# Kernel tuning notes

Hardware: AMD Instinct MI355X
Metric: run time of the kernel (lower is better)

The kernel has to match this reference:

```python
import jax, jax.numpy as jnp
import numpy as np
import math

UNIT = 46
KEY_SIZE = 16
MAX_POS = 50
NEG_BIG = 1.0e12


def _rope_tables(max_pos, d):
    pos = np.arange(max_pos, dtype=np.float32)[:, None]
    div = np.exp(np.arange(0, d, 2, dtype=np.float32) * (-math.log(10000.0) / d))
    sin = np.sin(pos * div)  # [P, d/2]
    cos = np.cos(pos * div)  # [P, d/2]
    # matches torch repeat_interleave(2, dim=-1) of the strided sinusoid table
    cos_rep = np.repeat(cos, 2, axis=-1)  # [P, d]
    sin_rep = np.repeat(sin, 2, axis=-1)  # [P, d]
    return jnp.asarray(cos_rep), jnp.asarray(sin_rep)

_COS, _SIN = _rope_tables(MAX_POS, KEY_SIZE)


def _apply_rope(qw):
    # qw: [B, S, d]
    s = qw.shape[-2]
    qw2 = jnp.stack([-qw[..., 1::2], qw[..., ::2]], axis=-1).reshape(qw.shape)
    return qw * _COS[:s] + qw2 * _SIN[:s]


def setup_inputs() -> dict:
    key = jax.random.key(0)
    ks = jax.random.split(key, 8)
    B, S = 32768, 50
    x = jax.random.normal(ks[0], (B, S, UNIT), dtype=jnp.float32)
    mask = jnp.ones((B, S), dtype=jnp.float32)
    d_in = UNIT
    sc = 1.0 / math.sqrt(d_in)
    Wi = jax.random.uniform(ks[1], (2 * UNIT + KEY_SIZE, d_in), minval=-sc, maxval=sc, dtype=jnp.float32)
    bi = jax.random.uniform(ks[2], (2 * UNIT + KEY_SIZE,), minval=-sc, maxval=sc, dtype=jnp.float32)
    Wo = jax.random.uniform(ks[3], (UNIT, UNIT), minval=-sc, maxval=sc, dtype=jnp.float32)
    bo = jax.random.uniform(ks[4], (UNIT,), minval=-sc, maxval=sc, dtype=jnp.float32)
    Wq = jax.random.uniform(ks[5], (1, UNIT), minval=-sc, maxval=sc, dtype=jnp.float32)
    bq = jax.random.uniform(ks[6], (1,), minval=-sc, maxval=sc, dtype=jnp.float32)
    scale_q = jnp.ones((KEY_SIZE,), jnp.float32)
    offset_q = jnp.zeros((KEY_SIZE,), jnp.float32)
    scale_k = jnp.ones((KEY_SIZE,), jnp.float32)
    offset_k = jnp.zeros((KEY_SIZE,), jnp.float32)
    return {"x": x, "mask": mask, "Wi": Wi, "bi": bi, "Wo": Wo, "bo": bo,
            "scale_q": scale_q, "offset_q": offset_q, "scale_k": scale_k,
            "offset_k": offset_k, "Wq": Wq, "bq": bq}


def reference(x, mask, Wi, bi, Wo, bo, scale_q, offset_q, scale_k, offset_k, Wq, bq):
    # x: [B, S, U], mask: [B, S]
    h = jax.nn.silu(jnp.einsum('bsu,ou->bso', x, Wi) + bi)  # [B, S, 2U+K]
    u, v, qk = jnp.split(h, [UNIT, 2 * UNIT], axis=-1)
    q = _apply_rope(qk * scale_q + offset_q)  # [B, S, K]
    k = _apply_rope(qk * scale_k + offset_k)  # [B, S, K]
    A = jnp.einsum('bik,bjk->bij', q, k) / math.sqrt(KEY_SIZE)  # [B, S, S]
    m = mask[:, None, :]
    A = jax.nn.softmax(A * m + (1.0 - m) * (-NEG_BIG), axis=-1)
    # NOTE: original overwrites the gated output with a plain matmul (u unused)
    out = jnp.einsum('bij,bju->biu', A, v)  # [B, S, U]
    out = jnp.einsum('biu,ou->bio', out, Wo) + bo  # [B, S, U]
    prob = (jnp.einsum('bsu,ou->bso', out, Wq) + bq)[..., 0]  # [B, S]
    prob = prob * mask - (1.0 - mask) * NEG_BIG
    prob = jax.nn.softmax(prob, axis=-1)
    return jnp.sum(out * prob[..., None], axis=1)  # [B, U]
```

## Files before the change

### kernel.cpp

```cpp
#include <hip/hip_runtime.h>
#include <math.h>

#define SEQ 50
#define UNITD 46
#define NEGBIG 1000000000000.0f

typedef _Float16 f16;
typedef f16 f16x4 __attribute__((ext_vector_type(4)));
typedef f16 f16x8 __attribute__((ext_vector_type(8)));
typedef float f32x4 __attribute__((ext_vector_type(4)));
typedef unsigned u32x2 __attribute__((ext_vector_type(2)));
typedef unsigned u32x4 __attribute__((ext_vector_type(4)));

__device__ __forceinline__ float rcpf(float x) { return __builtin_amdgcn_rcpf(x); }
__device__ __forceinline__ unsigned pk2(float lo, float hi) {
    return __builtin_bit_cast(unsigned, __builtin_amdgcn_cvt_pkrtz(lo, hi));
}

#define ARENA 12800
#define QOFF 0
#define KOFF 2560
#define VOFF 6400
#define MOFF 12544

__device__ __forceinline__ int swzP(int row, int colbyte) {
    return row * 128 + (colbyte ^ ((row & 7) << 4));
}
__device__ __forceinline__ int swzV(int row, int colbyte) {
    return VOFF + row * 128 + (colbyte ^ ((row & 7) << 4));
}

#define WS_ROPE 14336

__global__ void prep_kernel(const float* __restrict__ Wi,
                            const float* __restrict__ Wo,
                            char* __restrict__ ws)
{
    f16x8* wf = (f16x8*)ws;
    const int lane = threadIdx.x & 63;
    const int g = lane >> 4, t = lane & 15;
    #pragma unroll
    for (int nt = 0; nt < 4; ++nt) {
        int c = t + 16 * nt; bool cok = c < 62;
        const float* wr = Wi + (size_t)(UNITD + (cok ? c : 0)) * UNITD;
        #pragma unroll
        for (int kt = 0; kt < 2; ++kt) {
            f16x8 f;
            #pragma unroll
            for (int jj = 0; jj < 8; ++jj) {
                int u = 32 * kt + 8 * g + jj;
                f[jj] = (f16)((cok && u < UNITD) ? wr[u] : 0.f);
            }
            wf[(nt * 2 + kt) * 64 + lane] = f;
        }
    }
    #pragma unroll
    for (int mo = 0; mo < 3; ++mo) {
        int o = 16 * mo + t; bool ook = o < UNITD;
        const float* wr = Wo + (size_t)(ook ? o : 0) * UNITD;
        #pragma unroll
        for (int kt = 0; kt < 2; ++kt) {
            f16x8 f;
            #pragma unroll
            for (int jj = 0; jj < 8; ++jj) {
                int u = 32 * kt + 8 * g + jj;
                f[jj] = (f16)((ook && u < UNITD) ? wr[u] : 0.f);
            }
            wf[512 + (mo * 2 + kt) * 64 + lane] = f;
        }
    }
    {
        float2* rt = (float2*)(ws + WS_ROPE);
        int seq = threadIdx.x;
        #pragma unroll
        for (int d = 0; d < 16; ++d) {
            float ang = (float)seq * expf(-(float)(d >> 1) * 1.1512925464970229f);
            float sn, cs;
            sincosf(ang, &sn, &cs);
            float2 v; v.x = cs * 0.5f; v.y = ((d & 1) ? sn : -sn) * 0.5f;
            rt[seq * 16 + d] = v;
        }
    }
}

__global__ __launch_bounds__(256, 3) void gau_kernel(
    const float* __restrict__ x,
    const float* __restrict__ mask,
    const char* __restrict__ ws,
    const float* __restrict__ bi,
    const float* __restrict__ bo,
    const float* __restrict__ sq,
    const float* __restrict__ oq,
    const float* __restrict__ sk,
    const float* __restrict__ ok,
    const float* __restrict__ Wq,
    const float* __restrict__ bq,
    float* __restrict__ out,
    int Btot)
{
    const int lane = threadIdx.x & 63;
    const int wid  = threadIdx.x >> 6;
    const int b    = blockIdx.x * 4 + wid;
    const int g    = lane >> 4;
    const int t    = lane & 15;

    const f16x8* wf = (const f16x8*)ws;

    __shared__ __align__(16) char smem[4 * ARENA];
    char* wa = smem + wid * ARENA;
    float* M = (float*)(wa + MOFF);

    if (b >= Btot) return;

    M[lane] = (lane < SEQ) ? mask[(size_t)b * SEQ + lane] : 0.f;

    f16x8 bfW[4][2];
    float biv[4];
    #pragma unroll
    for (int nt = 0; nt < 4; ++nt) {
        int c = t + 16 * nt;
        biv[nt] = (c < 62) ? bi[UNITD + c] : 0.f;
        #pragma unroll
        for (int kt = 0; kt < 2; ++kt)
            bfW[nt][kt] = wf[(nt * 2 + kt) * 64 + lane];
    }

    f32x4 hB[4][4];
    #pragma unroll
    for (int mt = 0; mt < 4; ++mt)
        #pragma unroll
        for (int nt = 0; nt < 4; ++nt) {
            f32x4 c; c[0] = biv[nt]; c[1] = biv[nt]; c[2] = biv[nt]; c[3] = biv[nt];
            hB[mt][nt] = c;
        }

    const float* xb = x + (size_t)b * (SEQ * UNITD);
    #pragma unroll
    for (int mt = 0; mt < 4; ++mt) {
        int row = 16 * mt + t; if (row > SEQ - 1) row = SEQ - 1;
        const float* xr = xb + row * UNITD;
        #pragma unroll
        for (int kt = 0; kt < 2; ++kt) {
            u32x4 axw;
            #pragma unroll
            for (int jj2 = 0; jj2 < 4; ++jj2) {
                int u = 32 * kt + 8 * g + 2 * jj2;
                float lo = 0.f, hi = 0.f;
                if (u < UNITD) { float2 w = *(const float2*)(xr + u); lo = w.x; hi = w.y; }
                axw[jj2] = pk2(lo, hi);
            }
            f16x8 ax = __builtin_bit_cast(f16x8, axw);
            #pragma unroll
            for (int nt = 0; nt < 4; ++nt)
                hB[mt][nt] = __builtin_amdgcn_mfma_f32_16x16x32_f16(ax, bfW[nt][kt], hB[mt][nt], 0, 0, 0);
        }
    }

    float qkv[4][4];
    #pragma unroll
    for (int mt = 0; mt < 4; ++mt) {
        float s2[4], s3[4];
        #pragma unroll
        for (int nt = 0; nt < 4; ++nt) {
            float sl[4];
            #pragma unroll
            for (int r = 0; r < 4; ++r) {
                float h = hB[mt][nt][r];
                sl[r] = h * rcpf(1.f + __expf(-h));
            }
            int ucol = t + 16 * nt;
            if (nt < 3 && ucol < UNITD) {
                u32x2 pw; pw[0] = pk2(sl[0], sl[1]); pw[1] = pk2(sl[2], sl[3]);
                *(f16x4*)(wa + swzV(ucol, (16 * mt + 4 * g) * 2)) = __builtin_bit_cast(f16x4, pw);
            }
            if (nt == 2) { s2[0]=sl[0]; s2[1]=sl[1]; s2[2]=sl[2]; s2[3]=sl[3]; }
            if (nt == 3) { s3[0]=sl[0]; s3[1]=sl[1]; s3[2]=sl[2]; s3[3]=sl[3]; }
        }
        #pragma unroll
        for (int r = 0; r < 4; ++r) qkv[mt][r] = (t >= 14) ? s2[r] : s3[r];
    }

    {
        f16* Q = (f16*)(wa + QOFF);
        f16* K = (f16*)(wa + KOFF);
        const float2* rt = (const float2*)(ws + WS_ROPE);
        int d = (t >= 14) ? (t - 14) : (t + 2);
        float sqd = sq[d], oqd = oq[d], skd = sk[d], okd = ok[d];
        #pragma unroll
        for (int mt = 0; mt < 4; ++mt)
            #pragma unroll
            for (int r = 0; r < 4; ++r) {
                int seq = 16 * mt + 4 * g + r;
                float2 cn = rt[seq * 16 + d];
                float qv = qkv[mt][r] * sqd + oqd;
                float kv = qkv[mt][r] * skd + okd;
                float qp = __shfl_xor(qv, 1);
                float kp = __shfl_xor(kv, 1);
                Q[seq * 20 + d] = (f16)(qv * cn.x + qp * cn.y);
                K[seq * 20 + d] = (f16)(kv * cn.x + kp * cn.y);
            }
    }

    f16x4 ak[4], bq_[4];
    #pragma unroll
    for (int m4 = 0; m4 < 4; ++m4) ak[m4]  = *(f16x4*)(wa + KOFF + (16 * m4 + t) * 40 + 8 * g);
    #pragma unroll
    for (int n4 = 0; n4 < 4; ++n4) bq_[n4] = *(f16x4*)(wa + QOFF + (16 * n4 + t) * 40 + 8 * g);

    f32x4 pT[4][4];
    #pragma unroll
    for (int m4 = 0; m4 < 4; ++m4)
        #pragma unroll
        for (int n4 = 0; n4 < 4; ++n4) {
            f32x4 z; z[0]=0.f; z[1]=0.f; z[2]=0.f; z[3]=0.f;
            pT[m4][n4] = __builtin_amdgcn_mfma_f32_16x16x16f16(ak[m4], bq_[n4], z, 0, 0, 0);
        }

    f32x4 mj4[4];
    float NBv[4][4];
    #pragma unroll
    for (int m4 = 0; m4 < 4; ++m4) {
        mj4[m4] = *(f32x4*)(M + 16 * m4 + 4 * g);
        #pragma unroll
        for (int r = 0; r < 4; ++r)
            NBv[m4][r] = fmaf(mj4[m4][r], NEGBIG, -NEGBIG);
    }

    #pragma unroll
    for (int n4 = 0; n4 < 4; ++n4) {
        float a_[4][4];
        #pragma unroll
        for (int m4 = 0; m4 < 4; ++m4)
            #pragma unroll
            for (int r = 0; r < 4; ++r)
                a_[m4][r] = fmaf(pT[m4][n4][r], mj4[m4][r], NBv[m4][r]);

        float mr[4];
        #pragma unroll
        for (int m4 = 0; m4 < 4; ++m4)
            mr[m4] = fmaxf(fmaxf(a_[m4][0], a_[m4][1]), fmaxf(a_[m4][2], a_[m4][3]));
        float mx = fmaxf(fmaxf(mr[0], mr[1]), fmaxf(mr[2], mr[3]));
        mx = fmaxf(mx, __shfl_xor(mx, 16)); mx = fmaxf(mx, __shfl_xor(mx, 32));

        float sr[4];
        #pragma unroll
        for (int m4 = 0; m4 < 4; ++m4) {
            #pragma unroll
            for (int r = 0; r < 4; ++r) a_[m4][r] = __expf(a_[m4][r] - mx);
            sr[m4] = (a_[m4][0] + a_[m4][1]) + (a_[m4][2] + a_[m4][3]);
        }
        float sm = (sr[0] + sr[1]) + (sr[2] + sr[3]);
        sm += __shfl_xor(sm, 16); sm += __shfl_xor(sm, 32);
        float inv = rcpf(sm);

        int i = t + 16 * n4;
        if (i < SEQ) {
            #pragma unroll
            for (int m4 = 0; m4 < 4; ++m4) {
                u32x2 pw;
                pw[0] = pk2(a_[m4][0] * inv, a_[m4][1] * inv);
                pw[1] = pk2(a_[m4][2] * inv, a_[m4][3] * inv);
                *(f16x4*)(wa + swzP(i, (16 * m4 + 4 * g) * 2)) = __builtin_bit_cast(f16x4, pw);
            }
        }
    }

    f16x8 bv[3][2];
    #pragma unroll
    for (int nt = 0; nt < 3; ++nt)
        #pragma unroll
        for (int kt = 0; kt < 2; ++kt)
            bv[nt][kt] = *(f16x8*)(wa + swzV(t + 16 * nt, (32 * kt + 8 * g) * 2));

    f32x4 oA[4][3];
    #pragma unroll
    for (int mt = 0; mt < 4; ++mt)
        #pragma unroll
        for (int nt = 0; nt < 3; ++nt) { f32x4 z; z[0]=0.f; z[1]=0.f; z[2]=0.f; z[3]=0.f; oA[mt][nt] = z; }

    #pragma unroll
    for (int mt = 0; mt < 4; ++mt) {
        int pr = 16 * mt + t; if (pr > SEQ - 1) pr = SEQ - 1;
        #pragma unroll
        for (int kt = 0; kt < 2; ++kt) {
            f16x8 ap = *(f16x8*)(wa + swzP(pr, (32 * kt + 8 * g) * 2));
            #pragma unroll
            for (int nt = 0; nt < 3; ++nt)
                oA[mt][nt] = __builtin_amdgcn_mfma_f32_16x16x32_f16(ap, bv[nt][kt], oA[mt][nt], 0, 0, 0);
        }
    }

    #pragma unroll
    for (int mt = 0; mt < 4; ++mt)
        #pragma unroll
        for (int nt = 0; nt < 3; ++nt) {
            int u = t + 16 * nt;
            if (u < UNITD) {
                #pragma unroll
                for (int r = 0; r < 4; ++r) {
                    int i = 4 * g + r + 16 * mt;
                    if (i < SEQ)
                        *(f16*)(wa + swzP(i, u * 2)) = (f16)oA[mt][nt][r];
                }
            }
        }

    f16x8 aw[3][2];
    #pragma unroll
    for (int mo = 0; mo < 3; ++mo)
        #pragma unroll
        for (int kt = 0; kt < 2; ++kt)
            aw[mo][kt] = wf[512 + (mo * 2 + kt) * 64 + lane];

    float bov[3][4], wqv[3][4];
    #pragma unroll
    for (int mo = 0; mo < 3; ++mo)
        #pragma unroll
        for (int r = 0; r < 4; ++r) {
            int o = 16 * mo + 4 * g + r; bool ok2 = (o < UNITD);
            bov[mo][r] = ok2 ? bo[o] : 0.f;
            wqv[mo][r] = ok2 ? Wq[o] : 0.f;
        }

    f32x4 o2[3][4];
    #pragma unroll
    for (int mo = 0; mo < 3; ++mo)
        #pragma unroll
        for (int n4 = 0; n4 < 4; ++n4) {
            f32x4 c;
            #pragma unroll
            for (int r = 0; r < 4; ++r) c[r] = bov[mo][r];
            o2[mo][n4] = c;
        }

    #pragma unroll
    for (int n4 = 0; n4 < 4; ++n4) {
        int br = t + 16 * n4; if (br > SEQ - 1) br = SEQ - 1;
        #pragma unroll
        for (int kt = 0; kt < 2; ++kt) {
            f16x8 bo_ = *(f16x8*)(wa + swzP(br, (32 * kt + 8 * g) * 2));
            #pragma unroll
            for (int mo = 0; mo < 3; ++mo)
                o2[mo][n4] = __builtin_amdgcn_mfma_f32_16x16x32_f16(aw[mo][kt], bo_, o2[mo][n4], 0, 0, 0);
        }
    }

    float bq0 = bq[0];
    float tv[4]; float mx2 = -INFINITY;
    #pragma unroll
    for (int n4 = 0; n4 < 4; ++n4) {
        float s = 0.f;
        #pragma unroll
        for (int mo = 0; mo < 3; ++mo)
            #pragma unroll
            for (int r = 0; r < 4; ++r) s += o2[mo][n4][r] * wqv[mo][r];
        s += __shfl_xor(s, 16); s += __shfl_xor(s, 32);
        float mi = M[t + 16 * n4];
        float nb = fmaf(mi, NEGBIG, -NEGBIG);
        tv[n4] = fmaf(s + bq0, mi, nb);
        mx2 = fmaxf(mx2, tv[n4]);
    }
    #pragma unroll
    for (int off = 1; off <= 8; off <<= 1) mx2 = fmaxf(mx2, __shfl_xor(mx2, off));
    float sm2 = 0.f;
    #pragma unroll
    for (int n4 = 0; n4 < 4; ++n4) { float e = __expf(tv[n4] - mx2); tv[n4] = e; sm2 += e; }
    #pragma unroll
    for (int off = 1; off <= 8; off <<= 1) sm2 += __shfl_xor(sm2, off);
    float inv2 = rcpf(sm2);

    #pragma unroll
    for (int mo = 0; mo < 3; ++mo) {
        float racc[4];
        #pragma unroll
        for (int r = 0; r < 4; ++r) {
            float a = 0.f;
            #pragma unroll
            for (int n4 = 0; n4 < 4; ++n4) a += o2[mo][n4][r] * tv[n4];
            racc[r] = a;
        }
        #pragma unroll
        for (int off = 1; off <= 8; off <<= 1)
            #pragma unroll
            for (int r = 0; r < 4; ++r) racc[r] += __shfl_xor(racc[r], off);
        if (t == 0) {
            #pragma unroll
            for (int r = 0; r < 4; ++r) {
                int o = 16 * mo + 4 * g + r;
                if (o < UNITD) out[(size_t)b * UNITD + o] = racc[r] * inv2;
            }
        }
    }
}

extern "C" void kernel_launch(void* const* d_in, const int* in_sizes, int n_in,
                              void* d_out, int out_size, void* d_ws, size_t ws_size,
                              hipStream_t stream) {
    const float* x    = (const float*)d_in[0];
    const float* mask = (const float*)d_in[1];
    const float* Wi   = (const float*)d_in[2];
    const float* bi   = (const float*)d_in[3];
    const float* Wo   = (const float*)d_in[4];
    const float* bo   = (const float*)d_in[5];
    const float* sq   = (const float*)d_in[6];
    const float* oq   = (const float*)d_in[7];
    const float* sk   = (const float*)d_in[8];
    const float* ok   = (const float*)d_in[9];
    const float* Wq   = (const float*)d_in[10];
    const float* bq   = (const float*)d_in[11];
    float* outp       = (float*)d_out;

    prep_kernel<<<1, 64, 0, stream>>>(Wi, Wo, (char*)d_ws);

    const int B = in_sizes[0] / (SEQ * UNITD);
    const int blocks = (B + 3) / 4;
    gau_kernel<<<blocks, 256, 0, stream>>>(x, mask, (const char*)d_ws, bi, bo,
                                           sq, oq, sk, ok, Wq, bq, outp, B);
}
```

Measured before the change: 182.2 us.

## Split each batch element across two wavefronts with block-level sync

Each batch element is now processed by a pair of wavefronts instead of one, with each wave handling half of the sequence rows in the projection, attention and output stages. Shared-memory arenas are shared per pair, and the final softmax max/sum and weighted sums are combined through shared memory with several __syncthreads barriers. Launch bounds are raised to allow more resident blocks, aiming for lower register use and more parallelism per element. In exchange it adds block-wide barriers, duplicated weight and K fragment loads per wave, and padding writes of zeros for out-of-range V rows.

Result: slower. 298.1 us (+63.6%).

```diff
diff --git a/kernel.cpp b/kernel.cpp
--- a/kernel.cpp
+++ b/kernel.cpp
@@ -83,7 +83,7 @@
     }
 }
 
-__global__ __launch_bounds__(256, 3) void gau_kernel(
+__global__ __launch_bounds__(256, 6) void gau_kernel(
     const float* __restrict__ x,
     const float* __restrict__ mask,
     const char* __restrict__ ws,
@@ -100,19 +100,24 @@
 {
     const int lane = threadIdx.x & 63;
     const int wid  = threadIdx.x >> 6;
-    const int b    = blockIdx.x * 4 + wid;
+    const int pr_  = wid >> 1;
+    const int w    = wid & 1;
+    const int b    = blockIdx.x * 2 + pr_;
     const int g    = lane >> 4;
     const int t    = lane & 15;
 
     const f16x8* wf = (const f16x8*)ws;
 
-    __shared__ __align__(16) char smem[4 * ARENA];
-    char* wa = smem + wid * ARENA;
+    __shared__ __align__(16) char smem[2 * ARENA];
+    __shared__ float xmx[2][2], xsm[2][2];
+    __shared__ __align__(16) float xz[2][2][48];
+    char* wa = smem + pr_ * ARENA;
     float* M = (float*)(wa + MOFF);
 
-    if (b >= Btot) return;
-
-    M[lane] = (lane < SEQ) ? mask[(size_t)b * SEQ + lane] : 0.f;
+    const bool bok = (b < Btot);
+
+    if (bok && w == 0)
+        M[lane] = (lane < SEQ) ? mask[(size_t)b * SEQ + lane] : 0.f;
 
     f16x8 bfW[4][2];
     float biv[4];
@@ -125,95 +130,109 @@
             bfW[nt][kt] = wf[(nt * 2 + kt) * 64 + lane];
     }
 
-    f32x4 hB[4][4];
-    #pragma unroll
-    for (int mt = 0; mt < 4; ++mt)
+    f32x4 hB[2][4];
+    #pragma unroll
+    for (int mt2 = 0; mt2 < 2; ++mt2)
         #pragma unroll
         for (int nt = 0; nt < 4; ++nt) {
             f32x4 c; c[0] = biv[nt]; c[1] = biv[nt]; c[2] = biv[nt]; c[3] = biv[nt];
-            hB[mt][nt] = c;
-        }
-
-    const float* xb = x + (size_t)b * (SEQ * UNITD);
-    #pragma unroll
-    for (int mt = 0; mt < 4; ++mt) {
-        int row = 16 * mt + t; if (row > SEQ - 1) row = SEQ - 1;
-        const float* xr = xb + row * UNITD;
-        #pragma unroll
-        for (int kt = 0; kt < 2; ++kt) {
-            u32x4 axw;
-            #pragma unroll
-            for (int jj2 = 0; jj2 < 4; ++jj2) {
-                int u = 32 * kt + 8 * g + 2 * jj2;
-                float lo = 0.f, hi = 0.f;
-                if (u < UNITD) { float2 w = *(const float2*)(xr + u); lo = w.x; hi = w.y; }
-                axw[jj2] = pk2(lo, hi);
-            }
-            f16x8 ax = __builtin_bit_cast(f16x8, axw);
-            #pragma unroll
-            for (int nt = 0; nt < 4; ++nt)
-                hB[mt][nt] = __builtin_amdgcn_mfma_f32_16x16x32_f16(ax, bfW[nt][kt], hB[mt][nt], 0, 0, 0);
-        }
-    }
-
-    float qkv[4][4];
-    #pragma unroll
-    for (int mt = 0; mt < 4; ++mt) {
-        float s2[4], s3[4];
-        #pragma unroll
-        for (int nt = 0; nt < 4; ++nt) {
-            float sl[4];
-            #pragma unroll
-            for (int r = 0; r < 4; ++r) {
-                float h = hB[mt][nt][r];
-                sl[r] = h * rcpf(1.f + __expf(-h));
-            }
-            int ucol = t + 16 * nt;
-            if (nt < 3 && ucol < UNITD) {
-                u32x2 pw; pw[0] = pk2(sl[0], sl[1]); pw[1] = pk2(sl[2], sl[3]);
-                *(f16x4*)(wa + swzV(ucol, (16 * mt + 4 * g) * 2)) = __builtin_bit_cast(f16x4, pw);
-            }
-            if (nt == 2) { s2[0]=sl[0]; s2[1]=sl[1]; s2[2]=sl[2]; s2[3]=sl[3]; }
-            if (nt == 3) { s3[0]=sl[0]; s3[1]=sl[1]; s3[2]=sl[2]; s3[3]=sl[3]; }
-        }
-        #pragma unroll
-        for (int r = 0; r < 4; ++r) qkv[mt][r] = (t >= 14) ? s2[r] : s3[r];
-    }
-
-    {
-        f16* Q = (f16*)(wa + QOFF);
-        f16* K = (f16*)(wa + KOFF);
-        const float2* rt = (const float2*)(ws + WS_ROPE);
-        int d = (t >= 14) ? (t - 14) : (t + 2);
-        float sqd = sq[d], oqd = oq[d], skd = sk[d], okd = ok[d];
-        #pragma unroll
-        for (int mt = 0; mt < 4; ++mt)
-            #pragma unroll
-            for (int r = 0; r < 4; ++r) {
-                int seq = 16 * mt + 4 * g + r;
-                float2 cn = rt[seq * 16 + d];
-                float qv = qkv[mt][r] * sqd + oqd;
-                float kv = qkv[mt][r] * skd + okd;
-                float qp = __shfl_xor(qv, 1);
-                float kp = __shfl_xor(kv, 1);
-                Q[seq * 20 + d] = (f16)(qv * cn.x + qp * cn.y);
-                K[seq * 20 + d] = (f16)(kv * cn.x + kp * cn.y);
-            }
-    }
-
-    f16x4 ak[4], bq_[4];
-    #pragma unroll
-    for (int m4 = 0; m4 < 4; ++m4) ak[m4]  = *(f16x4*)(wa + KOFF + (16 * m4 + t) * 40 + 8 * g);
-    #pragma unroll
-    for (int n4 = 0; n4 < 4; ++n4) bq_[n4] = *(f16x4*)(wa + QOFF + (16 * n4 + t) * 40 + 8 * g);
-
-    f32x4 pT[4][4];
+            hB[mt2][nt] = c;
+        }
+
+    if (bok) {
+        const float* xb = x + (size_t)b * (SEQ * UNITD);
+        #pragma unroll
+        for (int mt2 = 0; mt2 < 2; ++mt2) {
+            int mt = 2 * w + mt2;
+            int row = 16 * mt + t; if (row > SEQ - 1) row = SEQ - 1;
+            const float* xr = xb + row * UNITD;
+            #pragma unroll
+            for (int kt = 0; kt < 2; ++kt) {
+                u32x4 axw;
+                #pragma unroll
+                for (int jj2 = 0; jj2 < 4; ++jj2) {
+                    int u = 32 * kt + 8 * g + 2 * jj2;
+                    float lo = 0.f, hi = 0.f;
+                    if (u < UNITD) { float2 ww = *(const float2*)(xr + u); lo = ww.x; hi = ww.y; }
+                    axw[jj2] = pk2(lo, hi);
+                }
+                f16x8 ax = __builtin_bit_cast(f16x8, axw);
+                #pragma unroll
+                for (int nt = 0; nt < 4; ++nt)
+                    hB[mt2][nt] = __builtin_amdgcn_mfma_f32_16x16x32_f16(ax, bfW[nt][kt], hB[mt2][nt], 0, 0, 0);
+            }
+        }
+
+        float qkv[2][4];
+        #pragma unroll
+        for (int mt2 = 0; mt2 < 2; ++mt2) {
+            int mt = 2 * w + mt2;
+            float s2[4], s3[4];
+            #pragma unroll
+            for (int nt = 0; nt < 4; ++nt) {
+                float sl[4];
+                #pragma unroll
+                for (int r = 0; r < 4; ++r) {
+                    float h = hB[mt2][nt][r];
+                    sl[r] = h * rcpf(1.f + __expf(-h));
+                }
+                int ucol = t + 16 * nt;
+                if (nt < 3 && ucol < UNITD) {
+                    int seqb = 16 * mt + 4 * g;
+                    float v0 = (seqb + 0 < SEQ) ? sl[0] : 0.f;
+                    float v1 = (seqb + 1 < SEQ) ? sl[1] : 0.f;
+                    float v2 = (seqb + 2 < SEQ) ? sl[2] : 0.f;
+                    float v3 = (seqb + 3 < SEQ) ? sl[3] : 0.f;
+                    u32x2 pw; pw[0] = pk2(v0, v1); pw[1] = pk2(v2, v3);
+                    *(f16x4*)(wa + swzV(ucol, seqb * 2)) = __builtin_bit_cast(f16x4, pw);
+                }
+                if (nt == 2) { s2[0]=sl[0]; s2[1]=sl[1]; s2[2]=sl[2]; s2[3]=sl[3]; }
+                if (nt == 3) { s3[0]=sl[0]; s3[1]=sl[1]; s3[2]=sl[2]; s3[3]=sl[3]; }
+            }
+            #pragma unroll
+            for (int r = 0; r < 4; ++r) qkv[mt2][r] = (t >= 14) ? s2[r] : s3[r];
+        }
+
+        {
+            f16* Q = (f16*)(wa + QOFF);
+            f16* K = (f16*)(wa + KOFF);
+            const float2* rt = (const float2*)(ws + WS_ROPE);
+            int d = (t >= 14) ? (t - 14) : (t + 2);
+            float sqd = sq[d], oqd = oq[d], skd = sk[d], okd = ok[d];
+            #pragma unroll
+            for (int mt2 = 0; mt2 < 2; ++mt2) {
+                int mt = 2 * w + mt2;
+                #pragma unroll
+                for (int r = 0; r < 4; ++r) {
+                    int seq = 16 * mt + 4 * g + r;
+                    float2 cn = rt[seq * 16 + d];
+                    float qv = qkv[mt2][r] * sqd + oqd;
+                    float kv = qkv[mt2][r] * skd + okd;
+                    float qp = __shfl_xor(qv, 1);
+                    float kp = __shfl_xor(kv, 1);
+                    Q[seq * 20 + d] = (f16)(qv * cn.x + qp * cn.y);
+                    K[seq * 20 + d] = (f16)(kv * cn.x + kp * cn.y);
+                }
+            }
+        }
+    }
+
+    __syncthreads();
+
+    f16x4 ak[4], bq_[2];
+    #pragma unroll
+    for (int m4 = 0; m4 < 4; ++m4) ak[m4] = *(f16x4*)(wa + KOFF + (16 * m4 + t) * 40 + 8 * g);
+    #pragma unroll
+    for (int n42 = 0; n42 < 2; ++n42)
+        bq_[n42] = *(f16x4*)(wa + QOFF + (16 * (2 * w + n42) + t) * 40 + 8 * g);
+
+    f32x4 pT[4][2];
     #pragma unroll
     for (int m4 = 0; m4 < 4; ++m4)
         #pragma unroll
-        for (int n4 = 0; n4 < 4; ++n4) {
+        for (int n42 = 0; n42 < 2; ++n42) {
             f32x4 z; z[0]=0.f; z[1]=0.f; z[2]=0.f; z[3]=0.f;
-            pT[m4][n4] = __builtin_amdgcn_mfma_f32_16x16x16f16(ak[m4], bq_[n4], z, 0, 0, 0);
+            pT[m4][n42] = __builtin_amdgcn_mfma_f32_16x16x16f16(ak[m4], bq_[n42], z, 0, 0, 0);
         }
 
     f32x4 mj4[4];
@@ -226,41 +245,45 @@
             NBv[m4][r] = fmaf(mj4[m4][r], NEGBIG, -NEGBIG);
     }
 
-    #pragma unroll
-    for (int n4 = 0; n4 < 4; ++n4) {
-        float a_[4][4];
-        #pragma unroll
-        for (int m4 = 0; m4 < 4; ++m4)
-            #pragma unroll
-            for (int r = 0; r < 4; ++r)
-                a_[m4][r] = fmaf(pT[m4][n4][r], mj4[m4][r], NBv[m4][r]);
-
-        float mr[4];
-        #pragma unroll
-        for (int m4 = 0; m4 < 4; ++m4)
-            mr[m4] = fmaxf(fmaxf(a_[m4][0], a_[m4][1]), fmaxf(a_[m4][2], a_[m4][3]));
-        float mx = fmaxf(fmaxf(mr[0], mr[1]), fmaxf(mr[2], mr[3]));
-        mx = fmaxf(mx, __shfl_xor(mx, 16)); mx = fmaxf(mx, __shfl_xor(mx, 32));
-
-        float sr[4];
-        #pragma unroll
-        for (int m4 = 0; m4 < 4; ++m4) {
-            #pragma unroll
-            for (int r = 0; r < 4; ++r) a_[m4][r] = __expf(a_[m4][r] - mx);
-            sr[m4] = (a_[m4][0] + a_[m4][1]) + (a_[m4][2] + a_[m4][3]);
-        }
-        float sm = (sr[0] + sr[1]) + (sr[2] + sr[3]);
-        sm += __shfl_xor(sm, 16); sm += __shfl_xor(sm, 32);
-        float inv = rcpf(sm);
-
-        int i = t + 16 * n4;
-        if (i < SEQ) {
+    __syncthreads();
+
+    if (bok) {
+        #pragma unroll
+        for (int n42 = 0; n42 < 2; ++n42) {
+            float a_[4][4];
+            #pragma unroll
+            for (int m4 = 0; m4 < 4; ++m4)
+                #pragma unroll
+                for (int r = 0; r < 4; ++r)
+                    a_[m4][r] = fmaf(pT[m4][n42][r], mj4[m4][r], NBv[m4][r]);
+
+            float mr[4];
+            #pragma unroll
+            for (int m4 = 0; m4 < 4; ++m4)
+                mr[m4] = fmaxf(fmaxf(a_[m4][0], a_[m4][1]), fmaxf(a_[m4][2], a_[m4][3]));
+            float mx = fmaxf(fmaxf(mr[0], mr[1]), fmaxf(mr[2], mr[3]));
+            mx = fmaxf(mx, __shfl_xor(mx, 16)); mx = fmaxf(mx, __shfl_xor(mx, 32));
+
+            float sr[4];
             #pragma unroll
             for (int m4 = 0; m4 < 4; ++m4) {
-                u32x2 pw;
-                pw[0] = pk2(a_[m4][0] * inv, a_[m4][1] * inv);
-                pw[1] = pk2(a_[m4][2] * inv, a_[m4][3] * inv);
-                *(f16x4*)(wa + swzP(i, (16 * m4 + 4 * g) * 2)) = __builtin_bit_cast(f16x4, pw);
+                #pragma unroll
+                for (int r = 0; r < 4; ++r) a_[m4][r] = __expf(a_[m4][r] - mx);
+                sr[m4] = (a_[m4][0] + a_[m4][1]) + (a_[m4][2] + a_[m4][3]);
+            }
+            float sm = (sr[0] + sr[1]) + (sr[2] + sr[3]);
+            sm += __shfl_xor(sm, 16); sm += __shfl_xor(sm, 32);
+            float inv = rcpf(sm);
+
+            int i = t + 16 * (2 * w + n42);
+            if (i < SEQ) {
+                #pragma unroll
+                for (int m4 = 0; m4 < 4; ++m4) {
+                    u32x2 pw;
+                    pw[0] = pk2(a_[m4][0] * inv, a_[m4][1] * inv);
+                    pw[1] = pk2(a_[m4][2] * inv, a_[m4][3] * inv);
+                    *(f16x4*)(wa + swzP(i, (16 * m4 + 4 * g) * 2)) = __builtin_bit_cast(f16x4, pw);
+                }
             }
         }
     }
@@ -272,38 +295,40 @@
         for (int kt = 0; kt < 2; ++kt)
             bv[nt][kt] = *(f16x8*)(wa + swzV(t + 16 * nt, (32 * kt + 8 * g) * 2));
 
-    f32x4 oA[4][3];
-    #pragma unroll
-    for (int mt = 0; mt < 4; ++mt)
-        #pragma unroll
-        for (int nt = 0; nt < 3; ++nt) { f32x4 z; z[0]=0.f; z[1]=0.f; z[2]=0.f; z[3]=0.f; oA[mt][nt] = z; }
-
-    #pragma unroll
-    for (int mt = 0; mt < 4; ++mt) {
-        int pr = 16 * mt + t; if (pr > SEQ - 1) pr = SEQ - 1;
-        #pragma unroll
-        for (int kt = 0; kt < 2; ++kt) {
-            f16x8 ap = *(f16x8*)(wa + swzP(pr, (32 * kt + 8 * g) * 2));
-            #pragma unroll
-            for (int nt = 0; nt < 3; ++nt)
-                oA[mt][nt] = __builtin_amdgcn_mfma_f32_16x16x32_f16(ap, bv[nt][kt], oA[mt][nt], 0, 0, 0);
-        }
-    }
-
-    #pragma unroll
-    for (int mt = 0; mt < 4; ++mt)
-        #pragma unroll
-        for (int nt = 0; nt < 3; ++nt) {
-            int u = t + 16 * nt;
-            if (u < UNITD) {
-                #pragma unroll
-                for (int r = 0; r < 4; ++r) {
-                    int i = 4 * g + r + 16 * mt;
-                    if (i < SEQ)
-                        *(f16*)(wa + swzP(i, u * 2)) = (f16)oA[mt][nt][r];
-                }
-            }
-        }
+    f32x4 oA[2][3];
+    #pragma unroll
+    for (int mt2 = 0; mt2 < 2; ++mt2)
+        #pragma unroll
+        for (int nt = 0; nt < 3; ++nt) { f32x4 z; z[0]=0.f; z[1]=0.f; z[2]=0.f; z[3]=0.f; oA[mt2][nt] = z; }
+
+    if (bok) {
+        #pragma unroll
+        for (int mt2 = 0; mt2 < 2; ++mt2) {
+            int pr = 16 * (2 * w + mt2) + t; if (pr > SEQ - 1) pr = SEQ - 1;
+            #pragma unroll
+            for (int kt = 0; kt < 2; ++kt) {
+                f16x8 ap = *(f16x8*)(wa + swzP(pr, (32 * kt + 8 * g) * 2));
+                #pragma unroll
+                for (int nt = 0; nt < 3; ++nt)
+                    oA[mt2][nt] = __builtin_amdgcn_mfma_f32_16x16x32_f16(ap, bv[nt][kt], oA[mt2][nt], 0, 0, 0);
+            }
+        }
+
+        #pragma unroll
+        for (int mt2 = 0; mt2 < 2; ++mt2)
+            #pragma unroll
+            for (int nt = 0; nt < 3; ++nt) {
+                int u = t + 16 * nt;
+                if (u < UNITD) {
+                    #pragma unroll
+                    for (int r = 0; r < 4; ++r) {
+                        int i = 4 * g + r + 16 * (2 * w + mt2);
+                        if (i < SEQ)
+                            *(f16*)(wa + swzP(i, u * 2)) = (f16)oA[mt2][nt][r];
+                    }
+                }
+            }
+    }
 
     f16x8 aw[3][2];
     #pragma unroll
@@ -322,72 +347,86 @@
             wqv[mo][r] = ok2 ? Wq[o] : 0.f;
         }
 
-    f32x4 o2[3][4];
+    f32x4 o2[3][2];
     #pragma unroll
     for (int mo = 0; mo < 3; ++mo)
         #pragma unroll
-        for (int n4 = 0; n4 < 4; ++n4) {
+        for (int n42 = 0; n42 < 2; ++n42) {
             f32x4 c;
             #pragma unroll
             for (int r = 0; r < 4; ++r) c[r] = bov[mo][r];
-            o2[mo][n4] = c;
-        }
-
-    #pragma unroll
-    for (int n4 = 0; n4 < 4; ++n4) {
-        int br = t + 16 * n4; if (br > SEQ - 1) br = SEQ - 1;
-        #pragma unroll
-        for (int kt = 0; kt < 2; ++kt) {
-            f16x8 bo_ = *(f16x8*)(wa + swzP(br, (32 * kt + 8 * g) * 2));
-            #pragma unroll
-            for (int mo = 0; mo < 3; ++mo)
-                o2[mo][n4] = __builtin_amdgcn_mfma_f32_16x16x32_f16(aw[mo][kt], bo_, o2[mo][n4], 0, 0, 0);
+            o2[mo][n42] = c;
+        }
+
+    if (bok) {
+        #pragma unroll
+        for (int n42 = 0; n42 < 2; ++n42) {
+            int br = t + 16 * (2 * w + n42); if (br > SEQ - 1) br = SEQ - 1;
+            #pragma unroll
+            for (int kt = 0; kt < 2; ++kt) {
+                f16x8 bo_ = *(f16x8*)(wa + swzP(br, (32 * kt + 8 * g) * 2));
+                #pragma unroll
+                for (int mo = 0; mo < 3; ++mo)
+                    o2[mo][n42] = __builtin_amdgcn_mfma_f32_16x16x32_f16(aw[mo][kt], bo_, o2[mo][n42], 0, 0, 0);
+            }
         }
     }
 
     float bq0 = bq[0];
-    float tv[4]; float mx2 = -INFINITY;
-    #pragma unroll
-    for (int n4 = 0; n4 < 4; ++n4) {
+    float tv[2];
+    #pragma unroll
+    for (int n42 = 0; n42 < 2; ++n42) {
         float s = 0.f;
         #pragma unroll
         for (int mo = 0; mo < 3; ++mo)
             #pragma unroll
-            for (int r = 0; r < 4; ++r) s += o2[mo][n4][r] * wqv[mo][r];
+            for (int r = 0; r < 4; ++r) s += o2[mo][n42][r] * wqv[mo][r];
         s += __shfl_xor(s, 16); s += __shfl_xor(s, 32);
-        float mi = M[t + 16 * n4];
+        float mi = M[t + 16 * (2 * w + n42)];
         float nb = fmaf(mi, NEGBIG, -NEGBIG);
-        tv[n4] = fmaf(s + bq0, mi, nb);
-        mx2 = fmaxf(mx2, tv[n4]);
-    }
-    #pragma unroll
-    for (int off = 1; off <= 8; off <<= 1) mx2 = fmaxf(mx2, __shfl_xor(mx2, off));
-    float sm2 = 0.f;
-    #pragma unroll
-    for (int n4 = 0; n4 < 4; ++n4) { float e = __expf(tv[n4] - mx2); tv[n4] = e; sm2 += e; }
-    #pragma unroll
-    for (int off = 1; off <= 8; off <<= 1) sm2 += __shfl_xor(sm2, off);
-    float inv2 = rcpf(sm2);
+        tv[n42] = fmaf(s + bq0, mi, nb);
+    }
+    float mxw = fmaxf(tv[0], tv[1]);
+    #pragma unroll
+    for (int off = 1; off <= 8; off <<= 1) mxw = fmaxf(mxw, __shfl_xor(mxw, off));
+    if (lane == 0) xmx[pr_][w] = mxw;
+    __syncthreads();
+    float mx2 = fmaxf(xmx[pr_][0], xmx[pr_][1]);
+    float e0 = __expf(tv[0] - mx2);
+    float e1 = __expf(tv[1] - mx2);
+    float smw = e0 + e1;
+    #pragma unroll
+    for (int off = 1; off <= 8; off <<= 1) smw += __shfl_xor(smw, off);
+    if (lane == 0) xsm[pr_][w] = smw;
+    __syncthreads();
+    float inv2 = rcpf(xsm[pr_][0] + xsm[pr_][1]);
 
     #pragma unroll
     for (int mo = 0; mo < 3; ++mo) {
-        float racc[4];
+        f32x4 racc;
         #pragma unroll
         for (int r = 0; r < 4; ++r) {
-            float a = 0.f;
-            #pragma unroll
-            for (int n4 = 0; n4 < 4; ++n4) a += o2[mo][n4][r] * tv[n4];
-            racc[r] = a;
+            float a = o2[mo][0][r] * e0;
+            a = fmaf(o2[mo][1][r], e1, a);
+            racc[r] = a * inv2;
         }
         #pragma unroll
         for (int off = 1; off <= 8; off <<= 1)
             #pragma unroll
             for (int r = 0; r < 4; ++r) racc[r] += __shfl_xor(racc[r], off);
-        if (t == 0) {
+        if (t == 0)
+            *(f32x4*)&xz[pr_][w][16 * mo + 4 * g] = racc;
+    }
+    __syncthreads();
+    if (bok && w == 0 && t == 0) {
+        #pragma unroll
+        for (int mo = 0; mo < 3; ++mo) {
+            f32x4 z0 = *(const f32x4*)&xz[pr_][0][16 * mo + 4 * g];
+            f32x4 z1 = *(const f32x4*)&xz[pr_][1][16 * mo + 4 * g];
             #pragma unroll
             for (int r = 0; r < 4; ++r) {
                 int o = 16 * mo + 4 * g + r;
-                if (o < UNITD) out[(size_t)b * UNITD + o] = racc[r] * inv2;
+                if (o < UNITD) out[(size_t)b * UNITD + o] = z0[r] + z1[r];
             }
         }
     }
@@ -413,7 +452,7 @@
     prep_kernel<<<1, 64, 0, stream>>>(Wi, Wo, (char*)d_ws);
 
     const int B = in_sizes[0] / (SEQ * UNITD);
-    const int blocks = (B + 3) / 4;
+    const int blocks = (B + 1) / 2;
     gau_kernel<<<blocks, 256, 0, stream>>>(x, mask, (const char*)d_ws, bi, bo,
                                            sq, oq, sk, ok, Wq, bq, outp, B);
 }
```
